# Kernel optimization log

Measured on AMD Instinct MI355X. Metric: run time of the kernel, lower is better.

The kernel has to match this reference:

```python
import jax, jax.numpy as jnp
import numpy as np

WINDOW = 100   # window_size
HEADS = 8      # num_heads
KDIM = 64      # Keras MHA key_dim (= value_dim by default)
D = 512        # model dim (query/key/value feature dim)
B = 8
L = 4096       # not a multiple of WINDOW -> pad_len = 4


def setup_inputs() -> dict:
    key = jax.random.key(0)
    ks = jax.random.split(key, 5)
    s = 0.02  # small init scale like glorot
    return {
        "x":  jax.random.normal(ks[0], (B, L, D), jnp.float32),
        "Wq": jax.random.normal(ks[1], (D, HEADS, KDIM), jnp.float32) * s,
        "bq": jnp.zeros((HEADS, KDIM), jnp.float32),
        "Wk": jax.random.normal(ks[2], (D, HEADS, KDIM), jnp.float32) * s,
        "bk": jnp.zeros((HEADS, KDIM), jnp.float32),
        "Wv": jax.random.normal(ks[3], (D, HEADS, KDIM), jnp.float32) * s,
        "bv": jnp.zeros((HEADS, KDIM), jnp.float32),
        "Wo": jax.random.normal(ks[4], (HEADS, KDIM, D), jnp.float32) * s,
        "bo": jnp.zeros((D,), jnp.float32),
    }


def reference(x, Wq, bq, Wk, bk, Wv, bv, Wo, bo):
    Bx, Lx, Dx = x.shape
    pad_len = (WINDOW - Lx % WINDOW) % WINDOW
    xp = jnp.pad(x, ((0, 0), (0, pad_len), (0, 0)))          # [B, L+pad, D]
    n_win = (Lx + pad_len) // WINDOW
    xw = xp.reshape(Bx * n_win, WINDOW, Dx)                  # [B*N, W, D]

    # Keras MultiHeadAttention(num_heads=HEADS, key_dim=KDIM), self-attention
    q = jnp.einsum('bwd,dhk->bwhk', xw, Wq) + bq             # [B*N, W, H, K]
    k = jnp.einsum('bwd,dhk->bwhk', xw, Wk) + bk
    v = jnp.einsum('bwd,dhk->bwhk', xw, Wv) + bv

    scale = 1.0 / np.sqrt(KDIM).astype(np.float32)
    scores = jnp.einsum('bqhk,bshk->bhqs', q, k) * scale     # [B*N, H, W, W]
    attn = jax.nn.softmax(scores, axis=-1)
    o = jnp.einsum('bhqs,bshk->bqhk', attn, v)               # [B*N, W, H, K]
    y = jnp.einsum('bqhk,hkd->bqd', o, Wo) + bo              # [B*N, W, D]

    return y.reshape(Bx, n_win, WINDOW, Dx)                  # pad_len is static (=4 here)
```

## Files before the change

kernel.cpp:

```cpp
#include <hip/hip_runtime.h>

typedef unsigned short u16;
typedef __attribute__((ext_vector_type(4))) float f32x4;
typedef __attribute__((ext_vector_type(8))) short short8;
typedef __attribute__((ext_vector_type(4))) short short4v;

#define WIN_SZ 100
#define NWIN 41
#define NBATCH 8
#define SEQ 4096
#define DM 512
#define NHEAD 8
#define KD 64
#define NWINS (NBATCH * NWIN)
#define MROWS (NWINS * WIN_SZ)
#define MBLKS 257
#define TOKPB (NWIN * WIN_SZ)
#define NQKV 1536
#define CONV_GRID 2048
#define GEMM_BLKS (((MBLKS + 7) / 8) * 32)

#define OFF_XBF   0u
#define OFF_OBUF  16793600u
#define OFF_WQKVT 33587200u
#define OFF_WOT   34373632u
#define OFF_ZBLK  34635776u
#define OFF_BIAS  34636032u
#define OFF_BIAS2 34639104u

#define MFMA16(a, b, c) __builtin_amdgcn_mfma_f32_16x16x16bf16_1k(a, b, c, 0, 0, 0)

__device__ __forceinline__ u16 f2bf(float f) {
  union { float f; unsigned i; } v; v.f = f;
  unsigned r = (v.i + 0x7fffu + ((v.i >> 16) & 1u)) >> 16;
  return (u16)r;
}

__device__ __forceinline__ unsigned cvt_pk_bf16(float a, float b) {
  unsigned r;
  asm("v_cvt_pk_bf16_f32 %0, %1, %2" : "=v"(r) : "v"(a), "v"(b));
  return r;
}

__device__ __forceinline__ float exp2_fast(float x) {
  float r;
  asm("v_exp_f32 %0, %1" : "=v"(r) : "v"(x));
  return r;
}

__device__ __forceinline__ void gl2lds16(const void* g, void* lds) {
  __builtin_amdgcn_global_load_lds(
      (const __attribute__((address_space(1))) void*)g,
      (__attribute__((address_space(3))) void*)lds, 16, 0, 0);
}

__global__ void prepx_k(const float* __restrict__ x,
                        const float* __restrict__ Wq, const float* __restrict__ Wk,
                        const float* __restrict__ Wv, const float* __restrict__ Wo,
                        const float* __restrict__ bq, const float* __restrict__ bk,
                        const float* __restrict__ bv, const float* __restrict__ bo,
                        u16* __restrict__ ws) {
  __shared__ u16 tile[64][65];
  const int t = threadIdx.x;
  if (blockIdx.x < CONV_GRID) {
    u16* xbf = ws + OFF_XBF;
    const int total = MROWS * 64;
    for (int i = blockIdx.x * 256 + t; i < total; i += CONV_GRID * 256) {
      int m = i >> 6;
      int c8 = (i & 63) * 8;
      int b = m / TOKPB, tk = m - b * TOKPB;
      uint4 ov = make_uint4(0u, 0u, 0u, 0u);
      if (tk < SEQ) {
        const float* src = x + (size_t)(b * SEQ + tk) * DM + c8;
        f32x4 v0 = __builtin_nontemporal_load((const f32x4*)src);
        f32x4 v1 = __builtin_nontemporal_load((const f32x4*)(src + 4));
        ov.x = cvt_pk_bf16(v0.x, v0.y);
        ov.y = cvt_pk_bf16(v0.z, v0.w);
        ov.z = cvt_pk_bf16(v1.x, v1.y);
        ov.w = cvt_pk_bf16(v1.z, v1.w);
      }
      *(uint4*)(xbf + (size_t)m * DM + c8) = ov;
    }
    return;
  }
  const int p = blockIdx.x - CONV_GRID;
  const int z = p >> 6, by = (p >> 3) & 7, bx = p & 7;
  const float* src = (z == 0) ? Wq : (z == 1) ? Wk : (z == 2) ? Wv : Wo;
  u16* dst = (z < 3) ? (ws + OFF_WQKVT + (unsigned)z * 512u * 512u)
                     : (ws + OFF_WOT);
  const int k0 = by * 64, n0 = bx * 64;
  const int c = t & 63, r4 = t >> 6;
#pragma unroll
  for (int pp = 0; pp < 16; ++pp) {
    int r = pp * 4 + r4;
    tile[r][c] = f2bf(src[(size_t)(k0 + r) * 512 + n0 + c]);
  }
  __syncthreads();
#pragma unroll
  for (int pp = 0; pp < 16; ++pp) {
    int r = pp * 4 + r4;
    dst[(size_t)(n0 + r) * 512 + k0 + c] = tile[c][r];
  }
  if (bx == 0 && by == 0) {
    float* biasF = (float*)(ws + OFF_BIAS);
    float* biasO = (float*)(ws + OFF_BIAS2);
    for (int j = t; j < 512; j += 256) {
      if (z == 0) biasF[j] = bq[j];
      else if (z == 1) biasF[512 + j] = bk[j];
      else if (z == 2) biasF[1024 + j] = bv[j];
      else biasO[j] = bo[j];
    }
    if (z == 3 && t < 128) ws[OFF_ZBLK + t] = 0;
  }
}

#define QKS 72
#define PS 136
#define SM_ELEMS 24832

__global__ __launch_bounds__(256, 3)
void qkvattn_k(const u16* __restrict__ ws) {
  __shared__ u16 smem[SM_ELEMS];
  u16* Xs  = smem;
  u16* Wsl = smem + 7168;
  u16* Vt  = smem;
  u16* Qs  = smem + 8704;
  u16* Ks  = smem + 16768;

  const int f = blockIdx.x;
  const int h = (f >> 3) & 7;
  const int win = ((f >> 6) << 3) + (f & 7);

  const int t = threadIdx.x, w = t >> 6, l = t & 63;
  const int q = l >> 4, cl = l & 15;
  const int lsw = (((t & 7) ^ ((t >> 3) & 7)) * 8);

  unsigned xoff[4];
#pragma unroll
  for (int i = 0; i < 4; ++i) {
    int m = i * 32 + (t >> 3);
    xoff[i] = (m < WIN_SZ)
                  ? (OFF_XBF + (unsigned)(win * WIN_SZ + m) * DM + lsw)
                  : OFF_ZBLK;
  }
  unsigned woff[6];
#pragma unroll
  for (int i = 0; i < 6; ++i) {
    int g = i * 32 + (t >> 3);
    unsigned nrow = (unsigned)(g >> 6) * 512u + (unsigned)h * 64u + (g & 63);
    woff[i] = OFF_WQKVT + nrow * DM + lsw;
  }

  f32x4 acc_p[7][3] = {};
  for (int k0 = 0; k0 < DM; k0 += 64) {
    __syncthreads();
#pragma unroll
    for (int i = 0; i < 4; ++i)
      if (i * 32 + w * 8 < 112)
        gl2lds16(ws + xoff[i] + (xoff[i] == OFF_ZBLK ? 0u : (unsigned)k0),
                 &Xs[(i * 32 + w * 8) * 64]);
#pragma unroll
    for (int i = 0; i < 6; ++i)
      gl2lds16(ws + woff[i] + k0, &Wsl[(i * 32 + w * 8) * 64]);
    __syncthreads();
#pragma unroll
    for (int ks = 0; ks < 2; ++ks) {
      const int ko = ks * 32 + q * 8;
      const int koS = ko ^ ((cl & 7) << 3);
      short8 af[7], bf[3];
#pragma unroll
      for (int mt = 0; mt < 7; ++mt)
        af[mt] = *(const short8*)&Xs[(mt * 16 + cl) * 64 + koS];
#pragma unroll
      for (int ntl = 0; ntl < 3; ++ntl)
        bf[ntl] = *(const short8*)&Wsl[((3 * w + ntl) * 16 + cl) * 64 + koS];
      __builtin_amdgcn_s_setprio(1);
#pragma unroll
      for (int mt = 0; mt < 7; ++mt)
#pragma unroll
        for (int ntl = 0; ntl < 3; ++ntl)
          acc_p[mt][ntl] = __builtin_amdgcn_mfma_f32_16x16x32_bf16(
              af[mt], bf[ntl], acc_p[mt][ntl], 0, 0, 0);
      __builtin_amdgcn_s_setprio(0);
    }
  }
  __syncthreads();

  {
    const float* biasF = (const float*)(ws + OFF_BIAS);
#pragma unroll
    for (int ntl = 0; ntl < 3; ++ntl) {
      const int nt = 3 * w + ntl;
      const int cw = (nt & 3) * 16 + cl;
      const float bb = biasF[(nt >> 2) * 512 + h * 64 + cw];
      if (nt < 8) {
        u16* dst = (nt < 4) ? Qs : Ks;
#pragma unroll
        for (int mt = 0; mt < 7; ++mt) {
          const int tok = mt * 16 + q * 4;
          unsigned p01 = cvt_pk_bf16(acc_p[mt][ntl][0] + bb, acc_p[mt][ntl][1] + bb);
          unsigned p23 = cvt_pk_bf16(acc_p[mt][ntl][2] + bb, acc_p[mt][ntl][3] + bb);
          dst[(tok + 0) * QKS + cw] = (u16)p01;
          dst[(tok + 1) * QKS + cw] = (u16)(p01 >> 16);
          dst[(tok + 2) * QKS + cw] = (u16)p23;
          dst[(tok + 3) * QKS + cw] = (u16)(p23 >> 16);
        }
      } else {
#pragma unroll
        for (int mt = 0; mt < 7; ++mt) {
          uint2 pv;
          pv.x = cvt_pk_bf16(acc_p[mt][ntl][0] + bb, acc_p[mt][ntl][1] + bb);
          pv.y = cvt_pk_bf16(acc_p[mt][ntl][2] + bb, acc_p[mt][ntl][3] + bb);
          *(uint2*)&Vt[cw * PS + mt * 16 + q * 4] = pv;
        }
      }
    }
  }
  __syncthreads();

  const int nmt = (w < 3) ? 2 : 1;
  const int mt0 = w, mt1 = w + 4;

  f32x4 accs[2][7];
#pragma unroll
  for (int im = 0; im < 2; ++im) {
    if (im < nmt) {
      const int mt = (im == 0) ? mt0 : mt1;
      const int ar = (mt * 16 + cl) * QKS + q * 8;
      short8 qa0 = *(const short8*)&Qs[ar];
      short8 qa1 = *(const short8*)&Qs[ar + 32];
      __builtin_amdgcn_s_setprio(1);
#pragma unroll
      for (int nt = 0; nt < 7; ++nt) {
        const int br = (nt * 16 + cl) * QKS + q * 8;
        short8 kb0 = *(const short8*)&Ks[br];
        short8 kb1 = *(const short8*)&Ks[br + 32];
        f32x4 c = {};
        c = __builtin_amdgcn_mfma_f32_16x16x32_bf16(kb0, qa0, c, 0, 0, 0);
        c = __builtin_amdgcn_mfma_f32_16x16x32_bf16(kb1, qa1, c, 0, 0, 0);
        accs[im][nt] = c;
      }
      __builtin_amdgcn_s_setprio(0);
    }
  }

  const float scale2 = 0.18033688011112042f;
  unsigned pk[2][7][2];
#pragma unroll
  for (int im = 0; im < 2; ++im) {
    if (im < nmt) {
      float mx = -1e30f;
#pragma unroll
      for (int nt = 0; nt < 7; ++nt)
#pragma unroll
        for (int r = 0; r < 4; ++r) {
          float s = accs[im][nt][r] * scale2;
          accs[im][nt][r] = s;
          if ((nt < 6) || (q == 0)) mx = fmaxf(mx, s);
        }
      mx = fmaxf(mx, __shfl_xor(mx, 16, 64));
      mx = fmaxf(mx, __shfl_xor(mx, 32, 64));
      float sum = 0.f;
#pragma unroll
      for (int nt = 0; nt < 7; ++nt)
#pragma unroll
        for (int r = 0; r < 4; ++r) {
          bool valid = (nt < 6) || (q == 0);
          float e = valid ? exp2_fast(accs[im][nt][r] - mx) : 0.f;
          accs[im][nt][r] = e;
          sum += e;
        }
      sum += __shfl_xor(sum, 16, 64);
      sum += __shfl_xor(sum, 32, 64);
      float inv = 1.0f / sum;
#pragma unroll
      for (int nt = 0; nt < 7; ++nt) {
        pk[im][nt][0] = cvt_pk_bf16(accs[im][nt][0] * inv, accs[im][nt][1] * inv);
        pk[im][nt][1] = cvt_pk_bf16(accs[im][nt][2] * inv, accs[im][nt][3] * inv);
      }
    }
  }

  f32x4 acco[2][4] = {};
  __builtin_amdgcn_s_setprio(1);
#pragma unroll
  for (int vt = 0; vt < 4; ++vt) {
#pragma unroll
    for (int nt = 0; nt < 7; ++nt) {
      short4v av = *(const short4v*)&Vt[(vt * 16 + cl) * PS + nt * 16 + q * 4];
      union { unsigned u[2]; short4v s; } b0, b1;
      b0.u[0] = pk[0][nt][0]; b0.u[1] = pk[0][nt][1];
      acco[0][vt] = MFMA16(av, b0.s, acco[0][vt]);
      if (nmt == 2) {
        b1.u[0] = pk[1][nt][0]; b1.u[1] = pk[1][nt][1];
        acco[1][vt] = MFMA16(av, b1.s, acco[1][vt]);
      }
    }
  }
  __builtin_amdgcn_s_setprio(0);

  u16* obuf = (u16*)(ws + OFF_OBUF);
  const size_t orow0 = (size_t)win * WIN_SZ;
#pragma unroll
  for (int im = 0; im < 2; ++im) {
    if (im < nmt) {
      const int mt = (im == 0) ? mt0 : mt1;
      const int row = mt * 16 + cl;
      if (row < WIN_SZ) {
#pragma unroll
        for (int vt = 0; vt < 4; ++vt) {
          uint2 ov;
          ov.x = cvt_pk_bf16(acco[im][vt][0], acco[im][vt][1]);
          ov.y = cvt_pk_bf16(acco[im][vt][2], acco[im][vt][3]);
          *(uint2*)&obuf[(orow0 + row) * DM + h * KD + vt * 16 + q * 4] = ov;
        }
      }
    }
  }
}

__global__ __launch_bounds__(256, 4)
void gemm_k(const u16* __restrict__ ws, unsigned aoff0, unsigned btoff,
            unsigned biasoff, float* __restrict__ Cout, int Ntot) {
  __shared__ u16 Alds[128 * 64];
  __shared__ u16 Blds[128 * 64];

  const int f = blockIdx.x;
  const int nb = (f >> 3) & 3;
  const int p = ((f >> 5) << 3) + (f & 7);
  if (p >= MBLKS) return;

  const int t = threadIdx.x;
  const int w = t >> 6;
  const int l = t & 63;
  const int m0 = p * 128, n0 = nb * 128;
  const int lr = t >> 3;
  const int lsw = (((t & 7) ^ ((t >> 3) & 7)) * 8);

  unsigned aoff[4], boff[4];
#pragma unroll
  for (int i = 0; i < 4; ++i) {
    int m = m0 + i * 32 + lr;
    aoff[i] = (m < MROWS) ? (aoff0 + (unsigned)m * DM + lsw) : OFF_ZBLK;
    boff[i] = btoff + (unsigned)(n0 + i * 32 + lr) * DM + lsw;
  }

  f32x4 acc[4][4] = {};
  const int wm = (w & 1) * 64;
  const int wn = (w >> 1) * 64;
  const int q = l >> 4, cl = l & 15;

  for (int k0 = 0; k0 < DM; k0 += 64) {
    __syncthreads();
#pragma unroll
    for (int i = 0; i < 4; ++i) {
      gl2lds16(ws + aoff[i] + (aoff[i] == OFF_ZBLK ? 0u : (unsigned)k0),
               &Alds[(i * 32 + w * 8) * 64]);
      gl2lds16(ws + boff[i] + k0, &Blds[(i * 32 + w * 8) * 64]);
    }
    __syncthreads();
#pragma unroll
    for (int ks = 0; ks < 2; ++ks) {
      short8 av[4], bv_[4];
      const int ko = ks * 32 + q * 8;
      const int koS = ko ^ ((cl & 7) << 3);
#pragma unroll
      for (int mi = 0; mi < 4; ++mi)
        av[mi] = *(const short8*)&Alds[(wm + mi * 16 + cl) * 64 + koS];
#pragma unroll
      for (int ni = 0; ni < 4; ++ni)
        bv_[ni] = *(const short8*)&Blds[(wn + ni * 16 + cl) * 64 + koS];
      __builtin_amdgcn_s_setprio(1);
#pragma unroll
      for (int mi = 0; mi < 4; ++mi)
#pragma unroll
        for (int ni = 0; ni < 4; ++ni)
          acc[mi][ni] = __builtin_amdgcn_mfma_f32_16x16x32_bf16(
              av[mi], bv_[ni], acc[mi][ni], 0, 0, 0);
      __builtin_amdgcn_s_setprio(0);
    }
  }

  const float* biasF = (const float*)(ws + biasoff);
#pragma unroll
  for (int mi = 0; mi < 4; ++mi) {
#pragma unroll
    for (int ni = 0; ni < 4; ++ni) {
      int col = n0 + wn + ni * 16 + cl;
      float bb = biasF[col];
#pragma unroll
      for (int r = 0; r < 4; ++r) {
        int row = m0 + wm + mi * 16 + q * 4 + r;
        if (row < MROWS)
          __builtin_nontemporal_store(acc[mi][ni][r] + bb,
                                      &Cout[(size_t)row * Ntot + col]);
      }
    }
  }
}

extern "C" void kernel_launch(void* const* d_in, const int* in_sizes, int n_in,
                              void* d_out, int out_size, void* d_ws, size_t ws_size,
                              hipStream_t stream) {
  const float* x  = (const float*)d_in[0];
  const float* Wq = (const float*)d_in[1];
  const float* bq = (const float*)d_in[2];
  const float* Wk = (const float*)d_in[3];
  const float* bk = (const float*)d_in[4];
  const float* Wv = (const float*)d_in[5];
  const float* bv = (const float*)d_in[6];
  const float* Wo = (const float*)d_in[7];
  const float* bo = (const float*)d_in[8];

  u16* ws = (u16*)d_ws;

  prepx_k<<<dim3(CONV_GRID + 256), dim3(256), 0, stream>>>(
      x, Wq, Wk, Wv, Wo, bq, bk, bv, bo, ws);
  qkvattn_k<<<dim3(NWINS * NHEAD), dim3(256), 0, stream>>>(ws);
  gemm_k<<<dim3(GEMM_BLKS), dim3(256), 0, stream>>>(
      ws, OFF_OBUF, OFF_WOT, OFF_BIAS2, (float*)d_out, DM);
}
```

Baseline: 236.7 us.

## Double-buffer GEMM LDS tiles with K=32 steps and prefetch next tile

Reworks the projection GEMM main loop to use two LDS buffers with a K step of 32 instead of 64. The loads for the next K slice are issued before the MFMAs on the current slice, leaving one barrier per iteration instead of two. The row-loading layout changes from a swizzled 64-wide layout to an unswizzled 32-wide one. This risks LDS bank conflicts on the reads and doubles the iteration count and barrier frequency.

```diff
diff --git a/kernel.cpp b/kernel.cpp
--- a/kernel.cpp
+++ b/kernel.cpp
@@ -322,63 +322,70 @@
 __global__ __launch_bounds__(256, 4)
 void gemm_k(const u16* __restrict__ ws, unsigned aoff0, unsigned btoff,
             unsigned biasoff, float* __restrict__ Cout, int Ntot) {
-  __shared__ u16 Alds[128 * 64];
-  __shared__ u16 Blds[128 * 64];
+  __shared__ u16 smg[2][8192];
 
   const int f = blockIdx.x;
   const int nb = (f >> 3) & 3;
   const int p = ((f >> 5) << 3) + (f & 7);
   if (p >= MBLKS) return;
 
-  const int t = threadIdx.x;
-  const int w = t >> 6;
-  const int l = t & 63;
+  const int t = threadIdx.x, w = t >> 6, l = t & 63;
   const int m0 = p * 128, n0 = nb * 128;
-  const int lr = t >> 3;
-  const int lsw = (((t & 7) ^ ((t >> 3) & 7)) * 8);
-
-  unsigned aoff[4], boff[4];
-#pragma unroll
-  for (int i = 0; i < 4; ++i) {
-    int m = m0 + i * 32 + lr;
-    aoff[i] = (m < MROWS) ? (aoff0 + (unsigned)m * DM + lsw) : OFF_ZBLK;
-    boff[i] = btoff + (unsigned)(n0 + i * 32 + lr) * DM + lsw;
+  const int q = l >> 4, cl = l & 15;
+
+  unsigned ssrc[4], smask[4], sdst[4];
+#pragma unroll
+  for (int j = 0; j < 4; ++j) {
+    const int id = w + j * 4;
+    if (id < 8) {
+      const int m = m0 + id * 16 + (l >> 2);
+      const bool real = (m < MROWS);
+      ssrc[j] = real ? (aoff0 + (unsigned)m * DM + (unsigned)(l & 3) * 8u) : OFF_ZBLK;
+      smask[j] = real ? 0xFFFFFFFFu : 0u;
+      sdst[j] = (unsigned)id * 512u;
+    } else {
+      const int n = n0 + (id - 8) * 16 + (l >> 2);
+      ssrc[j] = btoff + (unsigned)n * DM + (unsigned)(l & 3) * 8u;
+      smask[j] = 0xFFFFFFFFu;
+      sdst[j] = 4096u + (unsigned)(id - 8) * 512u;
+    }
   }
 
   f32x4 acc[4][4] = {};
   const int wm = (w & 1) * 64;
   const int wn = (w >> 1) * 64;
-  const int q = l >> 4, cl = l & 15;
-
-  for (int k0 = 0; k0 < DM; k0 += 64) {
+
+#pragma unroll
+  for (int j = 0; j < 4; ++j) gl2lds16(ws + ssrc[j], &smg[0][sdst[j]]);
+  __syncthreads();
+
+  for (int it = 0; it < 16; ++it) {
+    const int cur = it & 1;
+    if (it < 15) {
+      const unsigned k0n = (unsigned)(it + 1) * 32u;
+#pragma unroll
+      for (int j = 0; j < 4; ++j)
+        gl2lds16(ws + ssrc[j] + (k0n & smask[j]), &smg[cur ^ 1][sdst[j]]);
+    }
+    const u16* Ab = smg[cur];
+    const u16* Bb = Ab + 4096;
+    const int ko = q * 8;
+    short8 av[4], bv_[4];
+#pragma unroll
+    for (int mi = 0; mi < 4; ++mi)
+      av[mi] = *(const short8*)&Ab[(wm + mi * 16 + cl) * 32 + ko];
+#pragma unroll
+    for (int ni = 0; ni < 4; ++ni)
+      bv_[ni] = *(const short8*)&Bb[(wn + ni * 16 + cl) * 32 + ko];
+    __builtin_amdgcn_s_setprio(1);
+#pragma unroll
+    for (int mi = 0; mi < 4; ++mi)
+#pragma unroll
+      for (int ni = 0; ni < 4; ++ni)
+        acc[mi][ni] = __builtin_amdgcn_mfma_f32_16x16x32_bf16(
+            av[mi], bv_[ni], acc[mi][ni], 0, 0, 0);
+    __builtin_amdgcn_s_setprio(0);
     __syncthreads();
-#pragma unroll
-    for (int i = 0; i < 4; ++i) {
-      gl2lds16(ws + aoff[i] + (aoff[i] == OFF_ZBLK ? 0u : (unsigned)k0),
-               &Alds[(i * 32 + w * 8) * 64]);
-      gl2lds16(ws + boff[i] + k0, &Blds[(i * 32 + w * 8) * 64]);
-    }
-    __syncthreads();
-#pragma unroll
-    for (int ks = 0; ks < 2; ++ks) {
-      short8 av[4], bv_[4];
-      const int ko = ks * 32 + q * 8;
-      const int koS = ko ^ ((cl & 7) << 3);
-#pragma unroll
-      for (int mi = 0; mi < 4; ++mi)
-        av[mi] = *(const short8*)&Alds[(wm + mi * 16 + cl) * 64 + koS];
-#pragma unroll
-      for (int ni = 0; ni < 4; ++ni)
-        bv_[ni] = *(const short8*)&Blds[(wn + ni * 16 + cl) * 64 + koS];
-      __builtin_amdgcn_s_setprio(1);
-#pragma unroll
-      for (int mi = 0; mi < 4; ++mi)
-#pragma unroll
-        for (int ni = 0; ni < 4; ++ni)
-          acc[mi][ni] = __builtin_amdgcn_mfma_f32_16x16x32_bf16(
-              av[mi], bv_[ni], acc[mi][ni], 0, 0, 0);
-      __builtin_amdgcn_s_setprio(0);
-    }
   }
 
   const float* biasF = (const float*)(ws + biasoff);
```

Result: no change. 236.3 us (-0.2%).
